# Optimization experiments

Measured on AMD Instinct MI355X. Metric: run time of the kernel, lower is better.

## Reference

```python
import jax, jax.numpy as jnp
import numpy as np

N, DIM, HEADS, DH, WS = 32768, 1024, 8, 64, 256
INNER = HEADS * DH
MASK_VAL = -1e10  # ATTN_MASK_VALUE
EPS = 1e-5


def setup_inputs() -> dict:
    key = jax.random.key(0)
    k0, k1, k2 = jax.random.split(key, 3)
    x = jax.random.normal(k0, (N, DIM), jnp.float32)
    # rotary sin/cos with interleaved-pair layout matching rotate_every_two
    inv_freq = 1.0 / (10000.0 ** (jnp.arange(0, DH, 2, dtype=jnp.float32) / DH))
    freqs = jnp.arange(N, dtype=jnp.float32)[:, None] * inv_freq[None, :]  # [N, DH/2]
    sin = jnp.repeat(jnp.sin(freqs), 2, axis=-1)  # [N, DH]
    cos = jnp.repeat(jnp.cos(freqs), 2, axis=-1)  # [N, DH]
    gamma = jnp.ones((DIM,), jnp.float32)
    beta = jnp.zeros((DIM,), jnp.float32)
    w_qkv = jax.random.normal(k1, (DIM, 3 * INNER), jnp.float32) * 0.02
    w_out = jax.random.normal(k2, (INNER, DIM), jnp.float32) * 0.02
    b_out = jnp.zeros((DIM,), jnp.float32)
    return dict(x=x, sin=sin, cos=cos, gamma=gamma, beta=beta,
                w_qkv=w_qkv, w_out=w_out, b_out=b_out)


def _rotate_every_two(t):
    t1, t2 = t[..., 0::2], t[..., 1::2]
    return jnp.stack((-t2, t1), axis=-1).reshape(t.shape)


def _apply_rotary(t, sin, cos):
    # rot_dim == DH (full rotary), so no pass-through slice needed
    return t * cos + _rotate_every_two(t) * sin


def reference(x, sin, cos, gamma, beta, w_qkv, w_out, b_out):
    # LayerNorm (elementwise affine)
    mu = jnp.mean(x, axis=-1, keepdims=True)
    var = jnp.var(x, axis=-1, keepdims=True)
    x = (x - mu) * jax.lax.rsqrt(var + EPS) * gamma + beta
    # token shift: shift first half of channels by one token
    half = DIM // 2
    x_shift = jnp.pad(x[:, :half], ((1, 0), (0, 0)))[:-1]
    x = jnp.concatenate([x_shift, x[:, half:]], axis=-1)
    # qkv projection (no bias)
    qkv = x @ w_qkv  # [N, 3*INNER]
    q, k, v = jnp.split(qkv, 3, axis=-1)
    to_heads = lambda t: t.reshape(N, HEADS, DH).transpose(1, 0, 2)  # [H, N, DH]
    q, k, v = to_heads(q), to_heads(k), to_heads(v)
    # inline rotary on q, k AND v (as in source)
    q = _apply_rotary(q, sin, cos)
    k = _apply_rotary(k, sin, cos)
    v = _apply_rotary(v, sin, cos)
    # window split: [H, w, WS, DH]
    w = N // WS
    q, k, v = (t.reshape(HEADS, w, WS, DH) for t in (q, k, v))
    # look-back: each window attends to (previous window ++ current window)
    def lookback(t):
        t = jnp.pad(t, ((0, 0), (1, 0), (0, 0), (0, 0)))  # zero window at front
        return jnp.concatenate([t[:, :-1], t[:, 1:]], axis=2)  # [H, w, 2*WS, DH]
    k, v = lookback(k), lookback(v)
    sim = jnp.einsum('hwid,hwjd->hwij', q, k) * (DH ** -0.5)  # [H, w, WS, 2*WS]
    mask = jnp.tril(jnp.ones((WS, 2 * WS), dtype=bool), k=WS)  # j <= i + WS (causal)
    sim = jnp.where(mask, sim, MASK_VAL)
    attn = jax.nn.softmax(sim, axis=-1)
    out = jnp.einsum('hwij,hwjd->hwid', attn, v)  # [H, w, WS, DH]
    out = out.transpose(1, 2, 0, 3).reshape(N, INNER)  # '(w n) (h d)'
    return out @ w_out + b_out
```

## Files before the change

kernel.cpp:

```cpp
#include <hip/hip_runtime.h>

typedef __attribute__((ext_vector_type(4))) unsigned short us4;
typedef __attribute__((ext_vector_type(8))) unsigned short us8;
typedef __attribute__((ext_vector_type(8))) short s8;
typedef __attribute__((ext_vector_type(4))) float f32x4;
typedef __attribute__((ext_vector_type(16))) float f32x16;

#define NTOK 32768
#define DIM_ 1024
#define HEADS_ 8
#define DH_ 64
#define WS_ 256
#define NWIN_ 128
#define INNER_ 512

__device__ __forceinline__ float b2f(unsigned short u) {
  union { unsigned u; float f; } x; x.u = ((unsigned)u) << 16; return x.f;
}
__device__ __forceinline__ unsigned short f2b(float f) {
  union { float f; unsigned u; } x; x.f = f;
  unsigned r = x.u + 0x7FFFu + ((x.u >> 16) & 1u);
  return (unsigned short)(r >> 16);
}
__device__ __forceinline__ unsigned pk2(float a, float b) {
  return (unsigned)f2b(a) | ((unsigned)f2b(b) << 16);
}
__device__ __forceinline__ s8 mk_s8(unsigned w0, unsigned w1, unsigned w2, unsigned w3) {
  union { unsigned u[4]; s8 v; } x;
  x.u[0] = w0; x.u[1] = w1; x.u[2] = w2; x.u[3] = w3;
  return x.v;
}

__device__ __forceinline__ void gload_lds16(const unsigned short* g, void* l) {
  __builtin_amdgcn_global_load_lds((const __attribute__((address_space(1))) void*)g,
                                   (__attribute__((address_space(3))) void*)l, 16, 0, 0);
}

__global__ __launch_bounds__(256) void ln_shift(const float* __restrict__ x,
                                                const float* __restrict__ gamma,
                                                const float* __restrict__ beta,
                                                unsigned short* __restrict__ xs) {
  int row = blockIdx.x;
  int t = threadIdx.x;
  f32x4 v = ((const f32x4*)(x + (size_t)row * DIM_))[t];
  float sum = 0.f, ss = 0.f;
#pragma unroll
  for (int j = 0; j < 4; j++) { sum += v[j]; ss += v[j] * v[j]; }
#pragma unroll
  for (int off = 32; off >= 1; off >>= 1) {
    sum += __shfl_xor(sum, off);
    ss  += __shfl_xor(ss, off);
  }
  __shared__ float red[2][4];
  int wave = t >> 6, l = t & 63;
  if (l == 0) { red[0][wave] = sum; red[1][wave] = ss; }
  __syncthreads();
  sum = red[0][0] + red[0][1] + red[0][2] + red[0][3];
  ss  = red[1][0] + red[1][1] + red[1][2] + red[1][3];
  float mu = sum * (1.0f / DIM_);
  float var = ss * (1.0f / DIM_) - mu * mu;
  float rs = rsqrtf(var + 1e-5f);
  f32x4 g = ((const f32x4*)gamma)[t];
  f32x4 bb = ((const f32x4*)beta)[t];
  us4 o;
#pragma unroll
  for (int j = 0; j < 4; j++) o[j] = f2b((v[j] - mu) * rs * g[j] + bb[j]);
  int c0 = t * 4;
  if (c0 >= 512) {
    *(us4*)(xs + (size_t)row * DIM_ + c0) = o;
  } else {
    if (row + 1 < NTOK) *(us4*)(xs + (size_t)(row + 1) * DIM_ + c0) = o;
    if (row == 0) { us4 z = {0, 0, 0, 0}; *(us4*)(xs + c0) = z; }
  }
}

__global__ __launch_bounds__(256) void transpose_f32_bf16(const float* __restrict__ in,
                                                          unsigned short* __restrict__ out,
                                                          int R, int C) {
  __shared__ unsigned short tile[32][33];
  int bx = blockIdx.x * 32, by = blockIdx.y * 32;
  int tx = threadIdx.x, ty = threadIdx.y;
#pragma unroll
  for (int i = 0; i < 32; i += 8) tile[ty + i][tx] = f2b(in[(size_t)(by + ty + i) * C + bx + tx]);
  __syncthreads();
#pragma unroll
  for (int i = 0; i < 32; i += 8) out[(size_t)(bx + ty + i) * R + by + tx] = tile[tx][ty + i];
}

__device__ __forceinline__ void compute_tile64(const char* sa, const char* sb,
                                               f32x4 (&acc)[8][4],
                                               int wm, int wn, int ll, int lg) {
  s8 bf[4];
#pragma unroll
  for (int p = 0; p < 4; ++p) {
    const int qm = p & 1, kk = p >> 1;
    s8 af[4];
#pragma unroll
    for (int m = 0; m < 4; m++) {
      int r = wm * 128 + qm * 64 + m * 16 + ll;
      af[m] = *(const s8*)(sa + r * 128 + (((kk * 4 + lg) ^ (r & 7)) << 4));
    }
    if (qm == 0) {
#pragma unroll
      for (int n = 0; n < 4; n++) {
        int r = wn * 64 + n * 16 + ll;
        bf[n] = *(const s8*)(sb + r * 128 + (((kk * 4 + lg) ^ (r & 7)) << 4));
      }
    }
    __builtin_amdgcn_s_setprio(1);
#pragma unroll
    for (int m = 0; m < 4; m++)
#pragma unroll
      for (int n = 0; n < 4; n++)
        acc[qm * 4 + m][n] =
            __builtin_amdgcn_mfma_f32_16x16x32_bf16(af[m], bf[n], acc[qm * 4 + m][n], 0, 0, 0);
    __builtin_amdgcn_s_setprio(0);
  }
}

template <int MODE>
__global__ __launch_bounds__(512, 2) void gemm_p11(const unsigned short* __restrict__ A,
                                                   const unsigned short* __restrict__ Bt,
                                                   void* __restrict__ Cv,
                                                   const float* __restrict__ bias,
                                                   const float* __restrict__ sinp,
                                                   const float* __restrict__ cosp,
                                                   unsigned short* __restrict__ qh,
                                                   unsigned short* __restrict__ kh,
                                                   unsigned short* __restrict__ vt,
                                                   int M, int N, int K) {
  __shared__ __align__(16) char lds[163840];
  int t = threadIdx.x;
  int l = t & 63, lg = l >> 4, ll = l & 15;
  int wave = t >> 6;
  int wm = wave >> 2, wn = wave & 3;

  int nbx = gridDim.x;
  int nwg = nbx * gridDim.y;
  int flat = blockIdx.y * nbx + blockIdx.x;
  int swz = (flat & 7) * (nwg >> 3) + (flat >> 3);
  int m0 = (swz / nbx) * 256, n0 = (swz % nbx) * 256;

  const f32x4 fz = {0.f, 0.f, 0.f, 0.f};
  f32x4 acc[8][4];
#pragma unroll
  for (int m = 0; m < 8; m++)
#pragma unroll
    for (int n = 0; n < 4; n++) acc[m][n] = fz;

  int srow = t >> 3;
  int sunit = (t & 7) ^ (srow & 7);
  const unsigned short* gA = A + (size_t)(m0 + srow) * K + sunit * 8;
  const unsigned short* gB = Bt + (size_t)(n0 + srow) * K + sunit * 8;
  int t16 = t * 16;
  int nk = K >> 6;

#pragma unroll
  for (int j = 0; j < 4; j++) gload_lds16(gA + (size_t)(j * 64) * K, lds + j * 8192 + t16);
#pragma unroll
  for (int j = 0; j < 4; j++) gload_lds16(gB + (size_t)(j * 64) * K, lds + 98304 + j * 8192 + t16);
#pragma unroll
  for (int j = 0; j < 4; j++) gload_lds16(gA + 64 + (size_t)(j * 64) * K, lds + 32768 + j * 8192 + t16);

  for (int kt = 0; kt < nk - 2; ++kt) {
    const unsigned short* nB = gB + (kt + 1) * 64;
    char* dB = lds + 98304 + ((kt + 1) & 1) * 32768;
#pragma unroll
    for (int j = 0; j < 4; j++) gload_lds16(nB + (size_t)(j * 64) * K, dB + j * 8192 + t16);
    const unsigned short* nA = gA + (kt + 2) * 64;
    char* dA = lds + ((kt + 2) % 3) * 32768;
#pragma unroll
    for (int j = 0; j < 4; j++) gload_lds16(nA + (size_t)(j * 64) * K, dA + j * 8192 + t16);
    asm volatile("s_waitcnt vmcnt(12)" ::: "memory");
    __builtin_amdgcn_sched_barrier(0);
    __builtin_amdgcn_s_barrier();
    __builtin_amdgcn_sched_barrier(0);
    compute_tile64(lds + (kt % 3) * 32768, lds + 98304 + (kt & 1) * 32768, acc, wm, wn, ll, lg);
    __builtin_amdgcn_sched_barrier(0);
    __builtin_amdgcn_s_barrier();
  }
  {
    int kt = nk - 2;
    const unsigned short* nB = gB + (kt + 1) * 64;
    char* dB = lds + 98304 + ((kt + 1) & 1) * 32768;
#pragma unroll
    for (int j = 0; j < 4; j++) gload_lds16(nB + (size_t)(j * 64) * K, dB + j * 8192 + t16);
    asm volatile("s_waitcnt vmcnt(8)" ::: "memory");
    __builtin_amdgcn_sched_barrier(0);
    __builtin_amdgcn_s_barrier();
    __builtin_amdgcn_sched_barrier(0);
    compute_tile64(lds + (kt % 3) * 32768, lds + 98304 + (kt & 1) * 32768, acc, wm, wn, ll, lg);
    __builtin_amdgcn_sched_barrier(0);
    __builtin_amdgcn_s_barrier();
  }
  {
    int kt = nk - 1;
    asm volatile("s_waitcnt vmcnt(0)" ::: "memory");
    __builtin_amdgcn_sched_barrier(0);
    __builtin_amdgcn_s_barrier();
    __builtin_amdgcn_sched_barrier(0);
    compute_tile64(lds + (kt % 3) * 32768, lds + 98304 + (kt & 1) * 32768, acc, wm, wn, ll, lg);
  }

  if (MODE == 0) {
    int third = n0 >> 9;
    if (third == 2) {
      bool odd = (ll & 1) != 0;
#pragma unroll
      for (int m = 0; m < 8; m++) {
        int row0 = m0 + wm * 128 + m * 16 + lg * 4;
#pragma unroll
        for (int n = 0; n < 4; n++) {
          int cit = (n0 - 1024) + wn * 64 + n * 16 + ll;
          int head = cit >> 6, d = cit & 63;
          us4 st;
#pragma unroll
          for (int r = 0; r < 4; r++) {
            float v = acc[m][n][r];
            float p = __shfl_xor(v, 1);
            float sn = sinp[(size_t)(row0 + r) * 64 + d];
            float cs = cosp[(size_t)(row0 + r) * 64 + d];
            st[r] = f2b(odd ? (v * cs + p * sn) : (v * cs - p * sn));
          }
          *(us4*)(vt + ((size_t)head * 64 + d) * NTOK + row0) = st;
        }
      }
    } else {
      int b = ll & 3, q = ll >> 2;
      bool bo1 = (b & 1) != 0, bo2 = (b & 2) != 0;
#pragma unroll
      for (int m = 0; m < 8; m++) {
        int row = m0 + wm * 128 + m * 16 + lg * 4 + b;
#pragma unroll
        for (int n = 0; n < 4; n++) {
          float v0 = acc[m][n][0], v1 = acc[m][n][1], v2 = acc[m][n][2], v3 = acc[m][n][3];
          float x0 = __shfl_xor(v1, 1);
          float x1 = __shfl_xor(v0, 1);
          float x2 = __shfl_xor(v3, 1);
          float x3 = __shfl_xor(v2, 1);
          float u0 = bo1 ? x0 : v0;
          float u1 = bo1 ? v1 : x1;
          float u2 = bo1 ? x2 : v2;
          float u3 = bo1 ? v3 : x3;
          float y0 = __shfl_xor(u2, 2);
          float y1 = __shfl_xor(u3, 2);
          float y2 = __shfl_xor(u0, 2);
          float y3 = __shfl_xor(u1, 2);
          float w0 = bo2 ? y0 : u0;
          float w1 = bo2 ? y1 : u1;
          float w2 = bo2 ? u2 : y2;
          float w3 = bo2 ? u3 : y3;
          int cb = n0 + wn * 64 + n * 16 + q * 4;
          int cit = cb & 511;
          int head = cit >> 6, d0 = cit & 63;
          f32x4 s4 = *(const f32x4*)(sinp + (size_t)row * 64 + d0);
          f32x4 c4 = *(const f32x4*)(cosp + (size_t)row * 64 + d0);
          us4 st;
          st[0] = f2b(w0 * c4[0] - w1 * s4[0]);
          st[1] = f2b(w1 * c4[1] + w0 * s4[1]);
          st[2] = f2b(w2 * c4[2] - w3 * s4[2]);
          st[3] = f2b(w3 * c4[3] + w2 * s4[3]);
          if (third == 0) *(us4*)(qh + ((size_t)head * NTOK + row) * 64 + d0) = st;
          else            *(us4*)(kh + ((size_t)head * NTOK + row) * 64 + d0) = st;
        }
      }
    }
  } else {
#pragma unroll
    for (int n = 0; n < 4; n++) {
      int col = n0 + wn * 64 + n * 16 + ll;
      float bs = bias ? bias[col] : 0.0f;
#pragma unroll
      for (int m = 0; m < 8; m++) {
#pragma unroll
        for (int r = 0; r < 4; r++) {
          int row = m0 + wm * 128 + m * 16 + lg * 4 + r;
          ((float*)Cv)[(size_t)row * N + col] = acc[m][n][r] + bs;
        }
      }
    }
  }
}

__global__ __launch_bounds__(256, 4) void attn_kernel(const unsigned short* __restrict__ qh,
                                                      const unsigned short* __restrict__ kh,
                                                      const unsigned short* __restrict__ vt,
                                                      unsigned short* __restrict__ ao) {
  __shared__ char kbuf[2][8192];
  __shared__ char vbuf[8192];
  int half = blockIdx.x, w = blockIdx.y, h = blockIdx.z;
  int t = threadIdx.x;
  int wave = t >> 6, l = t & 63;
  int l31 = l & 31, hi = l >> 5;
  const unsigned short* qb = qh + (size_t)h * NTOK * 64;
  const unsigned short* kb = kh + (size_t)h * NTOK * 64;
  const unsigned short* vb = vt + (size_t)h * 64 * NTOK;

  int qw = half * 128 + wave * 32 + l31;
  int qn = w * 256 + qw;
  s8 qf[4];
#pragma unroll
  for (int dht = 0; dht < 4; dht++)
    qf[dht] = *(const s8*)(qb + (size_t)qn * 64 + dht * 16 + hi * 8);

  f32x16 o0 = {}, o1 = {};
  float dsum = (w == 0) ? 128.f : 0.f;
  int n0 = w * 256 - 256;
  int c0 = (w == 0) ? 4 : 0;

  int srow = wave * 16 + (l >> 3);
  int sunit = l & 7;

  {
    const unsigned short* g = kb + (size_t)(n0 + c0 * 64 + srow) * 64 + ((sunit ^ (srow & 7)) * 8);
    gload_lds16(g, kbuf[c0 & 1] + wave * 2048);
    gload_lds16(g + 8 * 64, kbuf[c0 & 1] + wave * 2048 + 1024);
  }
  __syncthreads();

  for (int c = c0; c < 8; ++c) {
    int cb = n0 + c * 64;
    {
      int d = srow;
      const unsigned short* g = vb + (size_t)d * NTOK + cb + ((sunit ^ (d & 7)) * 8);
      gload_lds16(g, vbuf + wave * 2048);
      gload_lds16(g + (size_t)8 * NTOK, vbuf + wave * 2048 + 1024);
    }
    if (c < 7) {
      const unsigned short* g = kb + (size_t)(cb + 64 + srow) * 64 + ((sunit ^ (srow & 7)) * 8);
      gload_lds16(g, kbuf[(c + 1) & 1] + wave * 2048);
      gload_lds16(g + 8 * 64, kbuf[(c + 1) & 1] + wave * 2048 + 1024);
    }

    f32x16 s[2] = {{}, {}};
    const char* kl = kbuf[c & 1];
#pragma unroll
    for (int kt = 0; kt < 2; kt++) {
#pragma unroll
      for (int dht = 0; dht < 4; dht++) {
        int row = kt * 32 + l31;
        int unit = (dht * 2 + hi) ^ (row & 7);
        s8 kf = *(const s8*)(kl + row * 128 + unit * 16);
        s[kt] = __builtin_amdgcn_mfma_f32_32x32x16_bf16(kf, qf[dht], s[kt], 0, 0, 0);
      }
    }

    unsigned P0[2][4], P1[2][4];
#pragma unroll
    for (int kt = 0; kt < 2; kt++) {
#pragma unroll
      for (int r = 0; r < 16; r++) {
        int j = c * 64 + kt * 32 + (r & 3) + 8 * (r >> 2) + hi * 4;
        float e = (j <= qw + 256) ? __expf(s[kt][r] * 0.125f) : 0.f;
        s[kt][r] = e;
        dsum += e;
      }
#pragma unroll
      for (int j2 = 0; j2 < 4; j2++) {
        P0[kt][j2] = pk2(s[kt][j2 * 4 + 0], s[kt][j2 * 4 + 1]);
        P1[kt][j2] = pk2(s[kt][j2 * 4 + 2], s[kt][j2 * 4 + 3]);
      }
    }

    __syncthreads();

#pragma unroll
    for (int tt = 0; tt < 4; tt++) {
      int kt = tt >> 1, ss = tt & 1;
      unsigned a = P0[kt][2 * ss], b = P1[kt][2 * ss];
      unsigned cx = P0[kt][2 * ss + 1], dx = P1[kt][2 * ss + 1];
      asm volatile("v_permlane32_swap_b32 %0, %1" : "+v"(a), "+v"(cx));
      asm volatile("v_permlane32_swap_b32 %0, %1" : "+v"(b), "+v"(dx));
      s8 pf = mk_s8(a, b, cx, dx);
      {
        int row = l31;
        int unit = (tt * 2 + hi) ^ (row & 7);
        s8 vf = *(const s8*)(vbuf + row * 128 + unit * 16);
        o0 = __builtin_amdgcn_mfma_f32_32x32x16_bf16(vf, pf, o0, 0, 0, 0);
      }
      {
        int row = 32 + l31;
        int unit = (tt * 2 + hi) ^ (row & 7);
        s8 vf = *(const s8*)(vbuf + row * 128 + unit * 16);
        o1 = __builtin_amdgcn_mfma_f32_32x32x16_bf16(vf, pf, o1, 0, 0, 0);
      }
    }
    __syncthreads();
  }

  dsum += __shfl_xor(dsum, 32);
  float inv = 1.f / dsum;

  unsigned short* orow = ao + (size_t)qn * INNER_ + h * 64;
#pragma unroll
  for (int g = 0; g < 4; g++) {
    us4 st0, st1;
#pragma unroll
    for (int rr = 0; rr < 4; rr++) {
      st0[rr] = f2b(o0[g * 4 + rr] * inv);
      st1[rr] = f2b(o1[g * 4 + rr] * inv);
    }
    *(us4*)(orow + g * 8 + hi * 4) = st0;
    *(us4*)(orow + 32 + g * 8 + hi * 4) = st1;
  }
}

extern "C" void kernel_launch(void* const* d_in, const int* in_sizes, int n_in,
                              void* d_out, int out_size, void* d_ws, size_t ws_size,
                              hipStream_t stream) {
  const float* x     = (const float*)d_in[0];
  const float* sin_  = (const float*)d_in[1];
  const float* cos_  = (const float*)d_in[2];
  const float* gamma = (const float*)d_in[3];
  const float* beta  = (const float*)d_in[4];
  const float* w_qkv = (const float*)d_in[5];
  const float* w_out = (const float*)d_in[6];
  const float* b_out = (const float*)d_in[7];

  char* ws = (char*)d_ws;
  const size_t OFF_WQT = 0;
  const size_t OFF_WOT = 3145728;
  const size_t OFF_XS  = 4194304;
  const size_t OFF_QH  = 71303168;
  const size_t OFF_KH  = 104857600;
  const size_t OFF_VT  = 138412032;
  const size_t NEEDED  = 171966464;
  if (ws_size < NEEDED) return;

  unsigned short* wqT = (unsigned short*)(ws + OFF_WQT);
  unsigned short* woT = (unsigned short*)(ws + OFF_WOT);
  unsigned short* xs  = (unsigned short*)(ws + OFF_XS);
  unsigned short* qh  = (unsigned short*)(ws + OFF_QH);
  unsigned short* kh  = (unsigned short*)(ws + OFF_KH);
  unsigned short* vt  = (unsigned short*)(ws + OFF_VT);
  unsigned short* ao  = xs;

  transpose_f32_bf16<<<dim3(1536 / 32, 1024 / 32), dim3(32, 8), 0, stream>>>(w_qkv, wqT, 1024, 1536);
  transpose_f32_bf16<<<dim3(1024 / 32, 512 / 32), dim3(32, 8), 0, stream>>>(w_out, woT, 512, 1024);
  ln_shift<<<NTOK, 256, 0, stream>>>(x, gamma, beta, xs);
  gemm_p11<0><<<dim3(1536 / 256, NTOK / 256), 512, 0, stream>>>(
      xs, wqT, nullptr, nullptr, sin_, cos_, qh, kh, vt, NTOK, 1536, 1024);
  attn_kernel<<<dim3(2, NWIN_, HEADS_), 256, 0, stream>>>(qh, kh, vt, ao);
  gemm_p11<1><<<dim3(1024 / 256, NTOK / 256), 512, 0, stream>>>(
      ao, woT, (void*)d_out, b_out, nullptr, nullptr, nullptr, nullptr, nullptr, NTOK, 1024, 512);
}
```

Measured before the change: 329.5 us.

## Interleave global prefetch issue with MFMA phases in GEMM main loop

Restructures the GEMM k-loop so the next B and A tile global-to-LDS loads are issued inside the first and second MFMA sub-phases instead of up front. Each of the four sub-phases now has its own barrier pair, and the vmcnt wait moves to the end of the last phase. This spreads memory issue across compute in a ping-pong style to hide load latency. In exchange it adds four times as many workgroup barriers per k-tile, and the correctness of the triple and double buffering now depends on the new wait placement.

```diff
diff --git a/kernel.cpp b/kernel.cpp
--- a/kernel.cpp
+++ b/kernel.cpp
@@ -87,39 +87,8 @@
   for (int i = 0; i < 32; i += 8) out[(size_t)(bx + ty + i) * R + by + tx] = tile[tx][ty + i];
 }
 
-__device__ __forceinline__ void compute_tile64(const char* sa, const char* sb,
-                                               f32x4 (&acc)[8][4],
-                                               int wm, int wn, int ll, int lg) {
-  s8 bf[4];
-#pragma unroll
-  for (int p = 0; p < 4; ++p) {
-    const int qm = p & 1, kk = p >> 1;
-    s8 af[4];
-#pragma unroll
-    for (int m = 0; m < 4; m++) {
-      int r = wm * 128 + qm * 64 + m * 16 + ll;
-      af[m] = *(const s8*)(sa + r * 128 + (((kk * 4 + lg) ^ (r & 7)) << 4));
-    }
-    if (qm == 0) {
-#pragma unroll
-      for (int n = 0; n < 4; n++) {
-        int r = wn * 64 + n * 16 + ll;
-        bf[n] = *(const s8*)(sb + r * 128 + (((kk * 4 + lg) ^ (r & 7)) << 4));
-      }
-    }
-    __builtin_amdgcn_s_setprio(1);
-#pragma unroll
-    for (int m = 0; m < 4; m++)
-#pragma unroll
-      for (int n = 0; n < 4; n++)
-        acc[qm * 4 + m][n] =
-            __builtin_amdgcn_mfma_f32_16x16x32_bf16(af[m], bf[n], acc[qm * 4 + m][n], 0, 0, 0);
-    __builtin_amdgcn_s_setprio(0);
-  }
-}
-
 template <int MODE>
-__global__ __launch_bounds__(512, 2) void gemm_p11(const unsigned short* __restrict__ A,
+__global__ __launch_bounds__(512, 2) void gemm_p12(const unsigned short* __restrict__ A,
                                                    const unsigned short* __restrict__ Bt,
                                                    void* __restrict__ Cv,
                                                    const float* __restrict__ bias,
@@ -161,45 +130,61 @@
   for (int j = 0; j < 4; j++) gload_lds16(gB + (size_t)(j * 64) * K, lds + 98304 + j * 8192 + t16);
 #pragma unroll
   for (int j = 0; j < 4; j++) gload_lds16(gA + 64 + (size_t)(j * 64) * K, lds + 32768 + j * 8192 + t16);
-
-  for (int kt = 0; kt < nk - 2; ++kt) {
-    const unsigned short* nB = gB + (kt + 1) * 64;
-    char* dB = lds + 98304 + ((kt + 1) & 1) * 32768;
-#pragma unroll
-    for (int j = 0; j < 4; j++) gload_lds16(nB + (size_t)(j * 64) * K, dB + j * 8192 + t16);
-    const unsigned short* nA = gA + (kt + 2) * 64;
-    char* dA = lds + ((kt + 2) % 3) * 32768;
-#pragma unroll
-    for (int j = 0; j < 4; j++) gload_lds16(nA + (size_t)(j * 64) * K, dA + j * 8192 + t16);
-    asm volatile("s_waitcnt vmcnt(12)" ::: "memory");
-    __builtin_amdgcn_sched_barrier(0);
-    __builtin_amdgcn_s_barrier();
-    __builtin_amdgcn_sched_barrier(0);
-    compute_tile64(lds + (kt % 3) * 32768, lds + 98304 + (kt & 1) * 32768, acc, wm, wn, ll, lg);
-    __builtin_amdgcn_sched_barrier(0);
-    __builtin_amdgcn_s_barrier();
-  }
-  {
-    int kt = nk - 2;
-    const unsigned short* nB = gB + (kt + 1) * 64;
-    char* dB = lds + 98304 + ((kt + 1) & 1) * 32768;
-#pragma unroll
-    for (int j = 0; j < 4; j++) gload_lds16(nB + (size_t)(j * 64) * K, dB + j * 8192 + t16);
-    asm volatile("s_waitcnt vmcnt(8)" ::: "memory");
-    __builtin_amdgcn_sched_barrier(0);
-    __builtin_amdgcn_s_barrier();
-    __builtin_amdgcn_sched_barrier(0);
-    compute_tile64(lds + (kt % 3) * 32768, lds + 98304 + (kt & 1) * 32768, acc, wm, wn, ll, lg);
-    __builtin_amdgcn_sched_barrier(0);
-    __builtin_amdgcn_s_barrier();
-  }
-  {
-    int kt = nk - 1;
-    asm volatile("s_waitcnt vmcnt(0)" ::: "memory");
-    __builtin_amdgcn_sched_barrier(0);
-    __builtin_amdgcn_s_barrier();
-    __builtin_amdgcn_sched_barrier(0);
-    compute_tile64(lds + (kt % 3) * 32768, lds + 98304 + (kt & 1) * 32768, acc, wm, wn, ll, lg);
+  asm volatile("s_waitcnt vmcnt(4)" ::: "memory");
+  __builtin_amdgcn_sched_barrier(0);
+  __builtin_amdgcn_s_barrier();
+
+  for (int kt = 0; kt < nk; ++kt) {
+    const char* sa = lds + (kt % 3) * 32768;
+    const char* sb = lds + 98304 + (kt & 1) * 32768;
+    s8 bf[4];
+#pragma unroll
+    for (int p = 0; p < 4; ++p) {
+      const int qm = p & 1, kk = p >> 1;
+      __builtin_amdgcn_sched_barrier(0);
+      s8 af[4];
+#pragma unroll
+      for (int m = 0; m < 4; m++) {
+        int r = wm * 128 + qm * 64 + m * 16 + ll;
+        af[m] = *(const s8*)(sa + r * 128 + (((kk * 4 + lg) ^ (r & 7)) << 4));
+      }
+      if (qm == 0) {
+#pragma unroll
+        for (int n = 0; n < 4; n++) {
+          int r = wn * 64 + n * 16 + ll;
+          bf[n] = *(const s8*)(sb + r * 128 + (((kk * 4 + lg) ^ (r & 7)) << 4));
+        }
+      }
+      if (p == 0 && kt + 1 < nk) {
+        const unsigned short* nB = gB + (kt + 1) * 64;
+        char* dB = lds + 98304 + ((kt + 1) & 1) * 32768;
+#pragma unroll
+        for (int j = 0; j < 4; j++) gload_lds16(nB + (size_t)(j * 64) * K, dB + j * 8192 + t16);
+      }
+      if (p == 1 && kt + 2 < nk) {
+        const unsigned short* nA = gA + (kt + 2) * 64;
+        char* dA = lds + ((kt + 2) % 3) * 32768;
+#pragma unroll
+        for (int j = 0; j < 4; j++) gload_lds16(nA + (size_t)(j * 64) * K, dA + j * 8192 + t16);
+      }
+      __builtin_amdgcn_sched_barrier(0);
+      __builtin_amdgcn_s_barrier();
+      __builtin_amdgcn_sched_barrier(0);
+      __builtin_amdgcn_s_setprio(1);
+#pragma unroll
+      for (int m = 0; m < 4; m++)
+#pragma unroll
+        for (int n = 0; n < 4; n++)
+          acc[qm * 4 + m][n] =
+              __builtin_amdgcn_mfma_f32_16x16x32_bf16(af[m], bf[n], acc[qm * 4 + m][n], 0, 0, 0);
+      __builtin_amdgcn_s_setprio(0);
+      if (p == 3) {
+        if (kt < nk - 2)       asm volatile("s_waitcnt vmcnt(4)" ::: "memory");
+        else if (kt == nk - 2) asm volatile("s_waitcnt vmcnt(0)" ::: "memory");
+      }
+      __builtin_amdgcn_sched_barrier(0);
+      __builtin_amdgcn_s_barrier();
+    }
   }
 
   if (MODE == 0) {
@@ -438,9 +423,9 @@
   transpose_f32_bf16<<<dim3(1536 / 32, 1024 / 32), dim3(32, 8), 0, stream>>>(w_qkv, wqT, 1024, 1536);
   transpose_f32_bf16<<<dim3(1024 / 32, 512 / 32), dim3(32, 8), 0, stream>>>(w_out, woT, 512, 1024);
   ln_shift<<<NTOK, 256, 0, stream>>>(x, gamma, beta, xs);
-  gemm_p11<0><<<dim3(1536 / 256, NTOK / 256), 512, 0, stream>>>(
+  gemm_p12<0><<<dim3(1536 / 256, NTOK / 256), 512, 0, stream>>>(
       xs, wqT, nullptr, nullptr, sin_, cos_, qh, kh, vt, NTOK, 1536, 1024);
   attn_kernel<<<dim3(2, NWIN_, HEADS_), 256, 0, stream>>>(qh, kh, vt, ao);
-  gemm_p11<1><<<dim3(1024 / 256, NTOK / 256), 512, 0, stream>>>(
+  gemm_p12<1><<<dim3(1024 / 256, NTOK / 256), 512, 0, stream>>>(
       ao, woT, (void*)d_out, b_out, nullptr, nullptr, nullptr, nullptr, nullptr, NTOK, 1024, 512);
 }
```

New measurement: 334.0 us. About the same (+1.4%).
